# Kernel tuning notes

Hardware: AMD Instinct MI355X
Metric: run time of the kernel (lower is better)

The kernel has to match this reference:

```python
import jax, jax.numpy as jnp
import numpy as np

KS = 3
N = KS * KS  # 9 kernel taps
EPS = 1e-5
LEAK = 0.1


def _conv2d(x, w, b=None, stride=1, pad=1):
    out = jax.lax.conv_general_dilated(
        x, w, (stride, stride), [(pad, pad), (pad, pad)],
        dimension_numbers=('NCHW', 'OIHW', 'NCHW'))
    if b is not None:
        out = out + b[None, :, None, None]
    return out


def setup_inputs() -> dict:
    key = jax.random.key(0)
    k1, k2, k3, k4 = jax.random.split(key, 4)
    b, c_in, c_out, H, W = 4, 128, 256, 128, 128
    x = jax.random.normal(k1, (b, c_in, H, W), dtype=jnp.float32)
    # offset-predicting conv (torch inits it to zero; small random keeps
    # sampling near-grid but nontrivial)
    p_w = jax.random.normal(k2, (2 * N, c_in, KS, KS), dtype=jnp.float32) * 0.01
    p_b = jnp.zeros((2 * N,), dtype=jnp.float32)
    # main conv weight (bias=False in DeformConv2d)
    w_conv = jax.random.normal(k3, (c_out, c_in, KS, KS), dtype=jnp.float32) * 0.05
    gamma = jnp.ones((c_out,), dtype=jnp.float32)
    beta = jnp.zeros((c_out,), dtype=jnp.float32)
    return {"x": x, "p_w": p_w, "p_b": p_b, "w_conv": w_conv,
            "gamma": gamma, "beta": beta}


def reference(x, p_w, p_b, w_conv, gamma, beta):
    b, c, H, W = x.shape
    # offsets: (b, 2N, H, W); first N channels = x-offsets, last N = y-offsets
    off = jnp.transpose(_conv2d(x, p_w, p_b), (0, 2, 3, 1))  # (b,h,w,2N)
    off_x, off_y = off[..., :N], off[..., N:]

    x_pad = jnp.pad(x, ((0, 0), (0, 0), (1, 1), (1, 1)))  # zero_padding(1)
    Hp, Wp = H + 2, W + 2

    # p = p_0 + p_n + offset (in padded coordinates)
    dx = jnp.repeat(jnp.arange(-1, 2), KS).astype(x.dtype)  # (9,)
    dy = jnp.tile(jnp.arange(-1, 2), KS).astype(x.dtype)
    p0x = jnp.arange(1, H + 1, dtype=x.dtype)[None, :, None, None]
    p0y = jnp.arange(1, W + 1, dtype=x.dtype)[None, None, :, None]
    px = p0x + dx + off_x  # (b,h,w,N)
    py = p0y + dy + off_y

    fx, fy = jnp.floor(px), jnp.floor(py)
    qlt_x = jnp.clip(fx, 0, Hp - 1)
    qlt_y = jnp.clip(fy, 0, Wp - 1)
    qrb_x = jnp.clip(fx + 1, 0, Hp - 1)
    qrb_y = jnp.clip(fy + 1, 0, Wp - 1)

    pcx = jnp.clip(px, 0, Hp - 1)
    pcy = jnp.clip(py, 0, Wp - 1)

    # bilinear weights (matches original g_lt/g_rb/g_lb/g_rt)
    g_lt = (1 + (qlt_x - pcx)) * (1 + (qlt_y - pcy))
    g_rb = (1 - (qrb_x - pcx)) * (1 - (qrb_y - pcy))
    g_lb = (1 + (qlt_x - pcx)) * (1 - (qrb_y - pcy))
    g_rt = (1 - (qrb_x - pcx)) * (1 + (qlt_y - pcy))

    x_flat = x_pad.reshape(b, c, Hp * Wp)
    ilt_x, ilt_y = qlt_x.astype(jnp.int32), qlt_y.astype(jnp.int32)
    irb_x, irb_y = qrb_x.astype(jnp.int32), qrb_y.astype(jnp.int32)

    def samp(ix, iy, g):
        idx = (ix * Wp + iy).reshape(b, -1)  # (b, h*w*N)
        v = jnp.take_along_axis(x_flat, idx[:, None, :], axis=2)
        return g[:, None] * v.reshape(b, c, H, W, N)

    x_off = (samp(ilt_x, ilt_y, g_lt) + samp(irb_x, irb_y, g_rb)
             + samp(ilt_x, irb_y, g_lb) + samp(irb_x, ilt_y, g_rt))

    # equivalent to reshaping to (b,c,3h,3w) and conv(k=3,s=3), bias=False
    out = jnp.einsum('bchwn,ocn->bohw', x_off,
                     w_conv.reshape(w_conv.shape[0], c, N))

    # BatchNorm2d (training-mode batch stats, biased var) + LeakyReLU(0.1)
    mean = out.mean(axis=(0, 2, 3), keepdims=True)
    var = ((out - mean) ** 2).mean(axis=(0, 2, 3), keepdims=True)
    out = (out - mean) * jax.lax.rsqrt(var + EPS)
    out = out * gamma[None, :, None, None] + beta[None, :, None, None]
    return jnp.where(out >= 0, out, LEAK * out)
```

## Files before the change

### kernel.cpp

```cpp
#include <hip/hip_runtime.h>
#include <cstdint>

typedef __attribute__((ext_vector_type(8))) short bf16x8;
typedef __attribute__((ext_vector_type(4))) float f32x4;

#define B_   4
#define C_   128
#define H_   128
#define W_   128
#define HP_  130
#define WP_  130
#define O_   256
#define HW_  (H_*W_)

#define XPAD_BYTES   (B_*HP_*WP_*C_*2)
#define OFF_BYTE     XPAD_BYTES
#define OFF_BYTES    (B_*HW_*18*4)
#define WREPB_BYTE   (OFF_BYTE + OFF_BYTES)
#define WREPB_BYTES  (9*C_*O_*2)
#define STATS_BYTE   (WREPB_BYTE + WREPB_BYTES)
#define WOFF_BYTE    (STATS_BYTE + 4096)
#define WOFF_BYTES   (9*4*4*32*8*2)

__device__ __forceinline__ unsigned pack_bf2(float a, float b) {
    unsigned ua = __builtin_bit_cast(unsigned, a) + 0x8000u;
    unsigned ub = __builtin_bit_cast(unsigned, b) + 0x8000u;
    return __builtin_amdgcn_perm(ub, ua, 0x07060302u);
}

__global__ void k_transpose(const float* __restrict__ x, unsigned short* __restrict__ xpad) {
    __shared__ float tile[32][33];
    int w0 = blockIdx.x * 32, c0 = blockIdx.y * 32;
    int bh = blockIdx.z;
    int b = bh >> 7, h = bh & 127;
    int tx = threadIdx.x, ty = threadIdx.y;
#pragma unroll
    for (int i = 0; i < 4; i++) {
        int c = c0 + ty + i * 8;
        tile[ty + i * 8][tx] = x[((b * C_ + c) * H_ + h) * W_ + w0 + tx];
    }
    __syncthreads();
    int tid = ty * 32 + tx;
    int cp = tid & 15;
    int wl = tid >> 4;
#pragma unroll
    for (int i = 0; i < 2; i++) {
        int wll = wl + i * 16;
        int w = w0 + wll;
        unsigned v = pack_bf2(tile[2 * cp][wll], tile[2 * cp + 1][wll]);
        *(unsigned*)(&xpad[((size_t)((b * HP_ + h + 1) * WP_ + (w + 1))) * C_ + c0 + 2 * cp]) = v;
    }
}

__global__ void k_repack2(const float* __restrict__ p_w, short* __restrict__ wofff) {
    int i = blockIdx.x * 256 + threadIdx.x;
    if (i < 9 * 4096) {
        int e = i & 7, m = (i >> 3) & 31, q = (i >> 8) & 3, kc = (i >> 10) & 3, tap = i >> 12;
        float f = (m < 18) ? p_w[((size_t)m * C_ + kc * 32 + q * 8 + e) * 9 + tap] : 0.f;
        unsigned u = __builtin_bit_cast(unsigned, f);
        u += 0x7fffu + ((u >> 16) & 1u);
        wofff[i] = (short)(u >> 16);
    }
}

__global__ __launch_bounds__(256) void k_offconv(const unsigned short* __restrict__ xpad,
                                                 const short* __restrict__ wofff,
                                                 const float* __restrict__ p_b,
                                                 float* __restrict__ offT) {
    int t = threadIdx.x;
    int ph = blockIdx.x;
    int h  = blockIdx.y;
    int b  = blockIdx.z;
    const unsigned short* xb = xpad + (size_t)b * HP_ * WP_ * C_;
    int lane = t & 63, wv = t >> 6;
    int q = lane >> 4, l15 = lane & 15;
    int pos0 = ph * 64 + wv * 16;
    int poscol = pos0 + l15;

    f32x4 accA = {0.f, 0.f, 0.f, 0.f}, accB = {0.f, 0.f, 0.f, 0.f};
    const bf16x8* Wf = (const bf16x8*)wofff;

    for (int tap = 0; tap < 9; tap++) {
        int row = h + tap / 3;
        int col = poscol + tap % 3;
        const unsigned short* src = xb + ((size_t)(row * WP_ + col)) * C_ + q * 8;
#pragma unroll
        for (int kc = 0; kc < 4; kc++) {
            bf16x8 a0 = Wf[(size_t)(((tap * 4 + kc) * 4 + q) * 32) + l15];
            bf16x8 a1 = Wf[(size_t)(((tap * 4 + kc) * 4 + q) * 32) + 16 + l15];
            bf16x8 bv = *(const bf16x8*)(src + kc * 32);
            accA = __builtin_amdgcn_mfma_f32_16x16x32_bf16(a0, bv, accA, 0, 0, 0);
            accB = __builtin_amdgcn_mfma_f32_16x16x32_bf16(a1, bv, accB, 0, 0, 0);
        }
    }
    size_t hw = (size_t)h * W_ + pos0 + l15;
#pragma unroll
    for (int r = 0; r < 4; r++) {
        int j = q * 4 + r;
        offT[((size_t)(b * 18 + j)) * HW_ + hw] = accA[r] + p_b[j];
    }
    if (q == 0) {
#pragma unroll
        for (int r = 0; r < 2; r++) {
            int j = 16 + r;
            offT[((size_t)(b * 18 + j)) * HW_ + hw] = accB[r] + p_b[j];
        }
    }
}

__global__ void k_repack(const float* __restrict__ w_conv, unsigned short* __restrict__ wrepb) {
    int i = blockIdx.x * 256 + threadIdx.x;
    if (i < 9 * C_ * O_) {
        int ki8 = i & 7;
        int o   = (i >> 3) & 255;
        int kq  = (i >> 11) & 3;
        int kc  = (i >> 13) & 3;
        int n   = i >> 15;
        int c = kc * 32 + kq * 8 + ki8;
        float f = w_conv[(o * C_ + c) * 9 + n];
        unsigned u = __builtin_bit_cast(unsigned, f);
        u += 0x7fffu + ((u >> 16) & 1u);
        wrepb[i] = (unsigned short)(u >> 16);
    }
}

__global__ __launch_bounds__(512, 4) void k_main(const unsigned short* __restrict__ xpad,
                                                 const float* __restrict__ offT,
                                                 const unsigned short* __restrict__ wrepb,
                                                 float* __restrict__ out,
                                                 float* __restrict__ stats) {
    __shared__ short Wl[8192];
    __shared__ short Vl[4128];
    __shared__ int   pbase[4][128];
    __shared__ float pg[4][128];
    __shared__ float red0[256], red1[256];
    __shared__ float slab[64 * 132];

    int t = threadIdx.x;
    int i_blk = blockIdx.x;
    int b = i_blk & 3;
    int h = i_blk >> 2;
    const unsigned short* xb = xpad + (size_t)b * HP_ * WP_ * C_;

    int lane = t & 63, wv = t >> 6;
    int q = lane >> 4, l15 = lane & 15;
    int m0 = (wv & 3) * 64;
    int ph = wv >> 2;
    int n0 = ph * 64;
    int c4g = t & 3, posb = t >> 2;

    f32x4 acc[4][4];
#pragma unroll
    for (int i = 0; i < 4; i++)
#pragma unroll
        for (int j = 0; j < 4; j++) acc[i][j] = (f32x4){0.f, 0.f, 0.f, 0.f};

    for (int n = 0; n < 9; n++) {
        __syncthreads();
        if (t < 128) {
            int w = t;
            float offx = offT[((size_t)(b * 18 + n)) * HW_ + h * W_ + w];
            float offy = offT[((size_t)(b * 18 + 9 + n)) * HW_ + h * W_ + w];
            int dxn = n / 3 - 1, dyn = n % 3 - 1;
            float px = (float)(h + 1 + dxn) + offx;
            float py = (float)(w + 1 + dyn) + offy;
            float pcx = fminf(fmaxf(px, 0.f), 129.f);
            float pcy = fminf(fmaxf(py, 0.f), 129.f);
            float fx = floorf(px), fy = floorf(py);
            float q0x = fminf(fmaxf(fx, 0.f), 129.f);
            float q0y = fminf(fmaxf(fy, 0.f), 129.f);
            float q1x = fminf(fmaxf(fx + 1.f, 0.f), 129.f);
            float q1y = fminf(fmaxf(fy + 1.f, 0.f), 129.f);
            float wx0 = 1.f + (q0x - pcx), wx1 = 1.f - (q1x - pcx);
            float wy0 = 1.f + (q0y - pcy), wy1 = 1.f - (q1y - pcy);
            int i0x = (int)q0x, i0y = (int)q0y, i1x = (int)q1x, i1y = (int)q1y;
            pbase[0][w] = (i0x * WP_ + i0y) * C_;
            pbase[1][w] = (i1x * WP_ + i1y) * C_;
            pbase[2][w] = (i0x * WP_ + i1y) * C_;
            pbase[3][w] = (i1x * WP_ + i0y) * C_;
            pg[0][w] = wx0 * wy0;
            pg[1][w] = wx1 * wy1;
            pg[2][w] = wx0 * wy1;
            pg[3][w] = wx1 * wy0;
        }
        for (int kc = 0; kc < 4; kc++) {
            __syncthreads();
            {
                const uint4* wsrc = (const uint4*)(wrepb + ((size_t)(n * 4 + kc)) * 8192);
                uint4* wd = (uint4*)Wl;
                wd[t] = wsrc[t];
                wd[t + 512] = wsrc[t + 512];
            }
            {
                int cof = kc * 32 + c4g * 8;
                int b0 = pbase[0][posb], b1 = pbase[1][posb], b2 = pbase[2][posb], b3 = pbase[3][posb];
                float g0 = pg[0][posb], g1 = pg[1][posb], g2 = pg[2][posb], g3 = pg[3][posb];
                uint4 A  = *(const uint4*)(xb + b0 + cof);
                uint4 Bv = *(const uint4*)(xb + b1 + cof);
                uint4 Cv = *(const uint4*)(xb + b2 + cof);
                uint4 Dv = *(const uint4*)(xb + b3 + cof);
                unsigned outw[4];
#pragma unroll
                for (int k = 0; k < 4; k++) {
                    unsigned ua = (&A.x)[k], ub = (&Bv.x)[k], uc = (&Cv.x)[k], ud = (&Dv.x)[k];
                    float alo = __builtin_bit_cast(float, ua << 16), ahi = __builtin_bit_cast(float, ua & 0xffff0000u);
                    float blo = __builtin_bit_cast(float, ub << 16), bhi = __builtin_bit_cast(float, ub & 0xffff0000u);
                    float clo = __builtin_bit_cast(float, uc << 16), chi = __builtin_bit_cast(float, uc & 0xffff0000u);
                    float dlo = __builtin_bit_cast(float, ud << 16), dhi = __builtin_bit_cast(float, ud & 0xffff0000u);
                    float vlo = g0 * alo + g1 * blo + g2 * clo + g3 * dlo;
                    float vhi = g0 * ahi + g1 * bhi + g2 * chi + g3 * dhi;
                    outw[k] = pack_bf2(vlo, vhi);
                }
                *(uint4*)&Vl[(size_t)(c4g * 129 + posb) * 8] = make_uint4(outw[0], outw[1], outw[2], outw[3]);
            }
            __syncthreads();
            {
                const bf16x8* Af = (const bf16x8*)Wl;
                const bf16x8* Bf = (const bf16x8*)Vl;
                bf16x8 av[4];
#pragma unroll
                for (int i = 0; i < 4; i++) av[i] = Af[q * 256 + m0 + i * 16 + l15];
#pragma unroll
                for (int j = 0; j < 4; j++) {
                    bf16x8 bv = Bf[q * 129 + n0 + j * 16 + l15];
#pragma unroll
                    for (int i = 0; i < 4; i++)
                        acc[i][j] = __builtin_amdgcn_mfma_f32_16x16x32_bf16(av[i], bv, acc[i][j], 0, 0, 0);
                }
            }
        }
    }

    __syncthreads();
    if (t < 256) { red0[t] = 0.f; red1[t] = 0.f; }
    __syncthreads();
#pragma unroll
    for (int i = 0; i < 4; i++) {
#pragma unroll
        for (int r = 0; r < 4; r++) {
            int o_loc = m0 + i * 16 + q * 4 + r;
            float s = 0.f, s2 = 0.f;
#pragma unroll
            for (int j = 0; j < 4; j++) { float v = acc[i][j][r]; s += v; s2 += v * v; }
            s  += __shfl_xor(s, 1);  s  += __shfl_xor(s, 2);  s  += __shfl_xor(s, 4);  s  += __shfl_xor(s, 8);
            s2 += __shfl_xor(s2, 1); s2 += __shfl_xor(s2, 2); s2 += __shfl_xor(s2, 4); s2 += __shfl_xor(s2, 8);
            if (l15 == 0) { atomicAdd(&red0[o_loc], s); atomicAdd(&red1[o_loc], s2); }
        }
    }
    __syncthreads();
    if (t < 256) {
        atomicAdd(&stats[t], red0[t]);
        atomicAdd(&stats[256 + t], red1[t]);
    }

    float* outb = out + ((size_t)b * O_) * HW_ + (size_t)h * W_;
#pragma unroll
    for (int i = 0; i < 4; i++) {
        __syncthreads();
        int o_rel_base = (wv & 3) * 16 + q * 4;
        int col_base = ph * 64 + l15;
#pragma unroll
        for (int j = 0; j < 4; j++)
#pragma unroll
            for (int r = 0; r < 4; r++)
                slab[(o_rel_base + r) * 132 + col_base + j * 16] = acc[i][j][r];
        __syncthreads();
#pragma unroll
        for (int pass = 0; pass < 4; pass++) {
            int f = pass * 512 + t;
            int ro = f >> 5, c4 = f & 31;
            int o = ((ro >> 4) << 6) + i * 16 + (ro & 15);
            float4 v = *(float4*)&slab[ro * 132 + c4 * 4];
            *(float4*)&outb[(size_t)o * HW_ + c4 * 4] = v;
        }
    }
}

__global__ void k_bnstats(float* __restrict__ stats,
                          const float* __restrict__ gamma,
                          const float* __restrict__ beta) {
    int t = threadIdx.x;
    float s = stats[t], s2 = stats[256 + t];
    float mean = s * (1.f / 65536.f);
    float var = s2 * (1.f / 65536.f) - mean * mean;
    float sc = gamma[t] * rsqrtf(var + 1e-5f);
    float sh = beta[t] - mean * sc;
    stats[512 + t] = sc;
    stats[768 + t] = sh;
}

__global__ __launch_bounds__(256) void k_apply(float* __restrict__ out,
                                               const float* __restrict__ stats) {
    int idx = blockIdx.x * 256 + threadIdx.x;
    int e = idx * 4;
    int o = (e >> 14) & 255;
    float sc = stats[512 + o], sh = stats[768 + o];
    float4 v = *(float4*)(out + e);
    v.x = v.x * sc + sh; v.x = (v.x >= 0.f) ? v.x : 0.1f * v.x;
    v.y = v.y * sc + sh; v.y = (v.y >= 0.f) ? v.y : 0.1f * v.y;
    v.z = v.z * sc + sh; v.z = (v.z >= 0.f) ? v.z : 0.1f * v.z;
    v.w = v.w * sc + sh; v.w = (v.w >= 0.f) ? v.w : 0.1f * v.w;
    *(float4*)(out + e) = v;
}

extern "C" void kernel_launch(void* const* d_in, const int* in_sizes, int n_in,
                              void* d_out, int out_size, void* d_ws, size_t ws_size,
                              hipStream_t stream) {
    const float* x      = (const float*)d_in[0];
    const float* p_w    = (const float*)d_in[1];
    const float* p_b    = (const float*)d_in[2];
    const float* w_conv = (const float*)d_in[3];
    const float* gamma  = (const float*)d_in[4];
    const float* beta   = (const float*)d_in[5];
    float* out = (float*)d_out;

    char* wsb = (char*)d_ws;
    unsigned short* xpad  = (unsigned short*)wsb;
    float*          offT  = (float*)(wsb + OFF_BYTE);
    unsigned short* wrepb = (unsigned short*)(wsb + WREPB_BYTE);
    float*          stats = (float*)(wsb + STATS_BYTE);
    short*          wofff = (short*)(wsb + WOFF_BYTE);

    hipMemsetAsync(xpad, 0, (size_t)XPAD_BYTES, stream);
    hipMemsetAsync(stats, 0, 4096, stream);

    k_transpose<<<dim3(W_ / 32, C_ / 32, B_ * H_), dim3(32, 8), 0, stream>>>(x, xpad);
    k_repack2<<<dim3(144), 256, 0, stream>>>(p_w, wofff);
    k_offconv<<<dim3(2, H_, B_), 256, 0, stream>>>(xpad, wofff, p_b, offT);
    k_repack<<<dim3((9 * C_ * O_ + 255) / 256), 256, 0, stream>>>(w_conv, wrepb);
    k_main<<<dim3(512), 512, 0, stream>>>(xpad, offT, wrepb, out, stats);
    k_bnstats<<<1, 256, 0, stream>>>(stats, gamma, beta);
    k_apply<<<dim3(16384), 256, 0, stream>>>(out, stats);
}
```

Measured before the change: 237.8 us.

## Double-buffer weight and sampled tiles with async global-to-LDS loads in deformable conv

```diff
diff --git a/kernel.cpp b/kernel.cpp
--- a/kernel.cpp
+++ b/kernel.cpp
@@ -21,6 +21,10 @@
 #define STATS_BYTE   (WREPB_BYTE + WREPB_BYTES)
 #define WOFF_BYTE    (STATS_BYTE + 4096)
 #define WOFF_BYTES   (9*4*4*32*8*2)
+
+typedef __attribute__((address_space(1))) const void gconst_void;
+typedef __attribute__((address_space(3))) void lds_void;
+#define GLD_LDS16(gp, lp) __builtin_amdgcn_global_load_lds((gconst_void*)(gp), (lds_void*)(lp), 16, 0, 0)
 
 __device__ __forceinline__ unsigned pack_bf2(float a, float b) {
     unsigned ua = __builtin_bit_cast(unsigned, a) + 0x8000u;
@@ -129,12 +133,11 @@
                                                  const unsigned short* __restrict__ wrepb,
                                                  float* __restrict__ out,
                                                  float* __restrict__ stats) {
-    __shared__ short Wl[8192];
-    __shared__ short Vl[4128];
-    __shared__ int   pbase[4][128];
-    __shared__ float pg[4][128];
+    __shared__ short Wl[2][8192];
+    __shared__ short Vl[2][4128];
+    __shared__ int   pbase[2][4][128];
+    __shared__ float pg[2][4][128];
     __shared__ float red0[256], red1[256];
-    __shared__ float slab[64 * 132];
 
     int t = threadIdx.x;
     int i_blk = blockIdx.x;
@@ -149,14 +152,7 @@
     int n0 = ph * 64;
     int c4g = t & 3, posb = t >> 2;
 
-    f32x4 acc[4][4];
-#pragma unroll
-    for (int i = 0; i < 4; i++)
-#pragma unroll
-        for (int j = 0; j < 4; j++) acc[i][j] = (f32x4){0.f, 0.f, 0.f, 0.f};
-
-    for (int n = 0; n < 9; n++) {
-        __syncthreads();
+    auto OFFSETS = [&](int n, int pb) {
         if (t < 128) {
             int w = t;
             float offx = offT[((size_t)(b * 18 + n)) * HW_ + h * W_ + w];
@@ -174,64 +170,110 @@
             float wx0 = 1.f + (q0x - pcx), wx1 = 1.f - (q1x - pcx);
             float wy0 = 1.f + (q0y - pcy), wy1 = 1.f - (q1y - pcy);
             int i0x = (int)q0x, i0y = (int)q0y, i1x = (int)q1x, i1y = (int)q1y;
-            pbase[0][w] = (i0x * WP_ + i0y) * C_;
-            pbase[1][w] = (i1x * WP_ + i1y) * C_;
-            pbase[2][w] = (i0x * WP_ + i1y) * C_;
-            pbase[3][w] = (i1x * WP_ + i0y) * C_;
-            pg[0][w] = wx0 * wy0;
-            pg[1][w] = wx1 * wy1;
-            pg[2][w] = wx0 * wy1;
-            pg[3][w] = wx1 * wy0;
-        }
-        for (int kc = 0; kc < 4; kc++) {
-            __syncthreads();
-            {
-                const uint4* wsrc = (const uint4*)(wrepb + ((size_t)(n * 4 + kc)) * 8192);
-                uint4* wd = (uint4*)Wl;
-                wd[t] = wsrc[t];
-                wd[t + 512] = wsrc[t + 512];
+            pbase[pb][0][w] = (i0x * WP_ + i0y) * C_;
+            pbase[pb][1][w] = (i1x * WP_ + i1y) * C_;
+            pbase[pb][2][w] = (i0x * WP_ + i1y) * C_;
+            pbase[pb][3][w] = (i1x * WP_ + i0y) * C_;
+            pg[pb][0][w] = wx0 * wy0;
+            pg[pb][1][w] = wx1 * wy1;
+            pg[pb][2][w] = wx0 * wy1;
+            pg[pb][3][w] = wx1 * wy0;
+        }
+    };
+
+    f32x4 acc[4][4];
+#pragma unroll
+    for (int i = 0; i < 4; i++)
+#pragma unroll
+        for (int j = 0; j < 4; j++) acc[i][j] = (f32x4){0.f, 0.f, 0.f, 0.f};
+
+    OFFSETS(0, 0);
+    __syncthreads();
+
+    {
+        const unsigned short* ws = wrepb;
+        GLD_LDS16(ws + (size_t)t * 8, &Wl[0][wv * 512]);
+        GLD_LDS16(ws + (size_t)(t + 512) * 8, &Wl[0][wv * 512 + 4096]);
+        int cof = c4g * 8;
+        uint4 A  = *(const uint4*)(xb + pbase[0][0][posb] + cof);
+        uint4 Bv = *(const uint4*)(xb + pbase[0][1][posb] + cof);
+        uint4 Cv = *(const uint4*)(xb + pbase[0][2][posb] + cof);
+        uint4 Dv = *(const uint4*)(xb + pbase[0][3][posb] + cof);
+        float g0 = pg[0][0][posb], g1 = pg[0][1][posb], g2 = pg[0][2][posb], g3 = pg[0][3][posb];
+        unsigned outw[4];
+#pragma unroll
+        for (int k = 0; k < 4; k++) {
+            unsigned ua = (&A.x)[k], ub = (&Bv.x)[k], uc = (&Cv.x)[k], ud = (&Dv.x)[k];
+            float alo = __builtin_bit_cast(float, ua << 16), ahi = __builtin_bit_cast(float, ua & 0xffff0000u);
+            float blo = __builtin_bit_cast(float, ub << 16), bhi = __builtin_bit_cast(float, ub & 0xffff0000u);
+            float clo = __builtin_bit_cast(float, uc << 16), chi = __builtin_bit_cast(float, uc & 0xffff0000u);
+            float dlo = __builtin_bit_cast(float, ud << 16), dhi = __builtin_bit_cast(float, ud & 0xffff0000u);
+            float vlo = g0 * alo + g1 * blo + g2 * clo + g3 * dlo;
+            float vhi = g0 * ahi + g1 * bhi + g2 * chi + g3 * dhi;
+            outw[k] = pack_bf2(vlo, vhi);
+        }
+        *(uint4*)&Vl[0][(unsigned)(c4g * 129 + posb) * 8] = make_uint4(outw[0], outw[1], outw[2], outw[3]);
+    }
+    __syncthreads();
+
+#pragma unroll 1
+    for (int s = 0; s < 36; s++) {
+        int cur = s & 1, nxt = cur ^ 1;
+        uint4 A, Bv, Cv, Dv;
+        float g0 = 0.f, g1 = 0.f, g2 = 0.f, g3 = 0.f;
+        bool st = (s < 35);
+        if (st) {
+            int s1 = s + 1;
+            const unsigned short* ws = wrepb + (size_t)s1 * 8192;
+            GLD_LDS16(ws + (size_t)t * 8, &Wl[nxt][wv * 512]);
+            GLD_LDS16(ws + (size_t)(t + 512) * 8, &Wl[nxt][wv * 512 + 4096]);
+            int n1 = s1 >> 2, kc1 = s1 & 3, pb1 = n1 & 1;
+            int cof = kc1 * 32 + c4g * 8;
+            A  = *(const uint4*)(xb + pbase[pb1][0][posb] + cof);
+            Bv = *(const uint4*)(xb + pbase[pb1][1][posb] + cof);
+            Cv = *(const uint4*)(xb + pbase[pb1][2][posb] + cof);
+            Dv = *(const uint4*)(xb + pbase[pb1][3][posb] + cof);
+            g0 = pg[pb1][0][posb]; g1 = pg[pb1][1][posb];
+            g2 = pg[pb1][2][posb]; g3 = pg[pb1][3][posb];
+        }
+        {
+            const bf16x8* Af = (const bf16x8*)Wl[cur];
+            const bf16x8* Bf = (const bf16x8*)Vl[cur];
+            bf16x8 av[4];
+#pragma unroll
+            for (int i = 0; i < 4; i++) av[i] = Af[q * 256 + m0 + i * 16 + l15];
+            __builtin_amdgcn_s_setprio(1);
+#pragma unroll
+            for (int j = 0; j < 4; j++) {
+                bf16x8 bv = Bf[q * 129 + n0 + j * 16 + l15];
+#pragma unroll
+                for (int i = 0; i < 4; i++)
+                    acc[i][j] = __builtin_amdgcn_mfma_f32_16x16x32_bf16(av[i], bv, acc[i][j], 0, 0, 0);
             }
-            {
-                int cof = kc * 32 + c4g * 8;
-                int b0 = pbase[0][posb], b1 = pbase[1][posb], b2 = pbase[2][posb], b3 = pbase[3][posb];
-                float g0 = pg[0][posb], g1 = pg[1][posb], g2 = pg[2][posb], g3 = pg[3][posb];
-                uint4 A  = *(const uint4*)(xb + b0 + cof);
-                uint4 Bv = *(const uint4*)(xb + b1 + cof);
-                uint4 Cv = *(const uint4*)(xb + b2 + cof);
-                uint4 Dv = *(const uint4*)(xb + b3 + cof);
-                unsigned outw[4];
-#pragma unroll
-                for (int k = 0; k < 4; k++) {
-                    unsigned ua = (&A.x)[k], ub = (&Bv.x)[k], uc = (&Cv.x)[k], ud = (&Dv.x)[k];
-                    float alo = __builtin_bit_cast(float, ua << 16), ahi = __builtin_bit_cast(float, ua & 0xffff0000u);
-                    float blo = __builtin_bit_cast(float, ub << 16), bhi = __builtin_bit_cast(float, ub & 0xffff0000u);
-                    float clo = __builtin_bit_cast(float, uc << 16), chi = __builtin_bit_cast(float, uc & 0xffff0000u);
-                    float dlo = __builtin_bit_cast(float, ud << 16), dhi = __builtin_bit_cast(float, ud & 0xffff0000u);
-                    float vlo = g0 * alo + g1 * blo + g2 * clo + g3 * dlo;
-                    float vhi = g0 * ahi + g1 * bhi + g2 * chi + g3 * dhi;
-                    outw[k] = pack_bf2(vlo, vhi);
-                }
-                *(uint4*)&Vl[(size_t)(c4g * 129 + posb) * 8] = make_uint4(outw[0], outw[1], outw[2], outw[3]);
+            __builtin_amdgcn_s_setprio(0);
+        }
+        if ((s & 3) == 2) {
+            int n = s >> 2;
+            if (n < 8) OFFSETS(n + 1, (n + 1) & 1);
+        }
+        if (st) {
+            unsigned outw[4];
+#pragma unroll
+            for (int k = 0; k < 4; k++) {
+                unsigned ua = (&A.x)[k], ub = (&Bv.x)[k], uc = (&Cv.x)[k], ud = (&Dv.x)[k];
+                float alo = __builtin_bit_cast(float, ua << 16), ahi = __builtin_bit_cast(float, ua & 0xffff0000u);
+                float blo = __builtin_bit_cast(float, ub << 16), bhi = __builtin_bit_cast(float, ub & 0xffff0000u);
+                float clo = __builtin_bit_cast(float, uc << 16), chi = __builtin_bit_cast(float, uc & 0xffff0000u);
+                float dlo = __builtin_bit_cast(float, ud << 16), dhi = __builtin_bit_cast(float, ud & 0xffff0000u);
+                float vlo = g0 * alo + g1 * blo + g2 * clo + g3 * dlo;
+                float vhi = g0 * ahi + g1 * bhi + g2 * chi + g3 * dhi;
+                outw[k] = pack_bf2(vlo, vhi);
             }
-            __syncthreads();
-            {
-                const bf16x8* Af = (const bf16x8*)Wl;
-                const bf16x8* Bf = (const bf16x8*)Vl;
-                bf16x8 av[4];
-#pragma unroll
-                for (int i = 0; i < 4; i++) av[i] = Af[q * 256 + m0 + i * 16 + l15];
-#pragma unroll
-                for (int j = 0; j < 4; j++) {
-                    bf16x8 bv = Bf[q * 129 + n0 + j * 16 + l15];
-#pragma unroll
-                    for (int i = 0; i < 4; i++)
-                        acc[i][j] = __builtin_amdgcn_mfma_f32_16x16x32_bf16(av[i], bv, acc[i][j], 0, 0, 0);
-                }
-            }
-        }
-    }
-
-    __syncthreads();
+            *(uint4*)&Vl[nxt][(unsigned)(c4g * 129 + posb) * 8] = make_uint4(outw[0], outw[1], outw[2], outw[3]);
+        }
+        __syncthreads();
+    }
+
     if (t < 256) { red0[t] = 0.f; red1[t] = 0.f; }
     __syncthreads();
 #pragma unroll
@@ -255,25 +297,16 @@
 
     float* outb = out + ((size_t)b * O_) * HW_ + (size_t)h * W_;
 #pragma unroll
-    for (int i = 0; i < 4; i++) {
-        __syncthreads();
-        int o_rel_base = (wv & 3) * 16 + q * 4;
-        int col_base = ph * 64 + l15;
-#pragma unroll
-        for (int j = 0; j < 4; j++)
-#pragma unroll
-            for (int r = 0; r < 4; r++)
-                slab[(o_rel_base + r) * 132 + col_base + j * 16] = acc[i][j][r];
-        __syncthreads();
-#pragma unroll
-        for (int pass = 0; pass < 4; pass++) {
-            int f = pass * 512 + t;
-            int ro = f >> 5, c4 = f & 31;
-            int o = ((ro >> 4) << 6) + i * 16 + (ro & 15);
-            float4 v = *(float4*)&slab[ro * 132 + c4 * 4];
-            *(float4*)&outb[(size_t)o * HW_ + c4 * 4] = v;
-        }
-    }
+    for (int i = 0; i < 4; i++)
+#pragma unroll
+        for (int j = 0; j < 4; j++) {
+            int col = ph * 64 + j * 16 + l15;
+#pragma unroll
+            for (int r = 0; r < 4; r++) {
+                int o = m0 + i * 16 + q * 4 + r;
+                outb[(size_t)o * HW_ + col] = acc[i][j][r];
+            }
+        }
 }
 
 __global__ void k_bnstats(float* __restrict__ stats,
```

Result: faster. 230.0 us (-3.3%).
